# Kernel optimization log

Measured on AMD Instinct MI355X. Metric: run time of the kernel, lower is better.

Reference implementation:

```python
import jax, jax.numpy as jnp
import numpy as np

N = 2048          # number of glyph samples
SRC = 64          # raw alpha map size
PAD = 32          # zero padding on each side -> 128x128 source
HIN = SRC + 2 * PAD   # 128
WIN = SRC + 2 * PAD   # 128
TH = SRC * 2      # target_h = 2 * targetsize (=64) -> 128
TW = SRC * 2


def setup_inputs() -> dict:
    key = jax.random.key(0)
    k1, k2, k3 = jax.random.split(key, 3)
    return {
        "affine_outs": jax.random.normal(k1, (N, 6), jnp.float32),
        "fill_alpha": jax.random.uniform(k2, (N, SRC, SRC), jnp.float32),
        "stroke_alpha": jax.random.uniform(k3, (N, SRC, SRC), jnp.float32),
        # all target sizes fixed to 64 (-> 128x128 output) for static shapes
        "targetsize": jnp.full((1, N, 2), SRC, jnp.int32),
    }


def _theta(affine_outs):
    # matches torch.split(affine_outs, 1, 1) ordering: 00,11,01,10,02,12
    a00 = jax.nn.sigmoid(affine_outs[:, 0]) * 2.0
    a11 = jax.nn.sigmoid(affine_outs[:, 1]) * 2.0
    a01 = jnp.tanh(affine_outs[:, 2]) * 2.0
    a10 = jnp.tanh(affine_outs[:, 3]) * 2.0
    a02 = jnp.tanh(affine_outs[:, 4])
    a12 = jnp.tanh(affine_outs[:, 5])
    row1 = jnp.stack([a00, a01, a02], axis=-1)  # [N,3]
    row2 = jnp.stack([a10, a11, a12], axis=-1)  # [N,3]
    return jnp.stack([row1, row2], axis=1)      # [N,2,3]


def _affine_grid(theta):
    # F.affine_grid align_corners=False base grid for (TH, TW)
    xs = (jnp.arange(TW, dtype=jnp.float32) + 0.5) * (2.0 / TW) - 1.0  # [TW]
    ys = (jnp.arange(TH, dtype=jnp.float32) + 0.5) * (2.0 / TH) - 1.0  # [TH]
    X = xs[None, :]  # broadcast to [TH,TW]
    Y = ys[:, None]
    t = theta[:, :, :, None, None]  # [N,2,3,1,1]
    gx = t[:, 0, 0] * X + t[:, 0, 1] * Y + t[:, 0, 2]  # [N,TH,TW]
    gy = t[:, 1, 0] * X + t[:, 1, 1] * Y + t[:, 1, 2]
    return gx, gy


def _bilinear_zeros(img, ix, iy):
    # grid_sample(mode='bilinear', padding_mode='zeros', align_corners=False)
    n = img.shape[0]
    b = jnp.arange(n)[:, None, None]
    x0 = jnp.floor(ix)
    y0 = jnp.floor(iy)
    wx = ix - x0
    wy = iy - y0

    def fetch(xf, yf):
        xi = jnp.clip(xf, 0, WIN - 1).astype(jnp.int32)
        yi = jnp.clip(yf, 0, HIN - 1).astype(jnp.int32)
        v = img[b, yi, xi]
        valid = (xf >= 0) & (xf <= WIN - 1) & (yf >= 0) & (yf <= HIN - 1)
        return jnp.where(valid, v, 0.0)

    return (fetch(x0, y0) * (1 - wx) * (1 - wy)
            + fetch(x0 + 1, y0) * wx * (1 - wy)
            + fetch(x0, y0 + 1) * (1 - wx) * wy
            + fetch(x0 + 1, y0 + 1) * wx * wy)


def reference(affine_outs, fill_alpha, stroke_alpha, targetsize):
    theta = _theta(affine_outs)
    gx, gy = _affine_grid(theta)
    # normalized -> pixel coords (align_corners=False)
    ix = ((gx + 1.0) * WIN - 1.0) * 0.5
    iy = ((gy + 1.0) * HIN - 1.0) * 0.5
    pad = ((0, 0), (PAD, PAD), (PAD, PAD))
    fill_p = jnp.pad(fill_alpha, pad)
    stroke_p = jnp.pad(stroke_alpha, pad)
    fill_out = _bilinear_zeros(fill_p, ix, iy)      # [N,TH,TW]
    stroke_out = _bilinear_zeros(stroke_p, ix, iy)  # [N,TH,TW]
    return fill_out, stroke_out
```

## Files before the change

kernel.cpp:

```cpp
#include <hip/hip_runtime.h>

#define N_IMG 2048
#define SRC   64
#define PADW  32
#define HIN   128
#define WIN   128
#define TH    128
#define TW    128

__global__ __launch_bounds__(256) void affine_sample_kernel(
    const float* __restrict__ affine,
    const float* __restrict__ fill,
    const float* __restrict__ stroke,
    float* __restrict__ out)
{
    __shared__ float sF[SRC * SRC];
    __shared__ float sS[SRC * SRC];

    const int n = blockIdx.x;
    const float* __restrict__ fptr = fill   + (size_t)n * SRC * SRC;
    const float* __restrict__ sptr = stroke + (size_t)n * SRC * SRC;

    for (int i = threadIdx.x; i < SRC * SRC / 4; i += 256) {
        reinterpret_cast<float4*>(sF)[i] = reinterpret_cast<const float4*>(fptr)[i];
        reinterpret_cast<float4*>(sS)[i] = reinterpret_cast<const float4*>(sptr)[i];
    }

    const float t0 = affine[n * 6 + 0];
    const float t1 = affine[n * 6 + 1];
    const float t2 = affine[n * 6 + 2];
    const float t3 = affine[n * 6 + 3];
    const float t4 = affine[n * 6 + 4];
    const float t5 = affine[n * 6 + 5];
    const float a00 = 2.0f / (1.0f + expf(-t0));
    const float a11 = 2.0f / (1.0f + expf(-t1));
    const float a01 = 2.0f * tanhf(t2);
    const float a10 = 2.0f * tanhf(t3);
    const float a02 = tanhf(t4);
    const float a12 = tanhf(t5);

    __syncthreads();

    float* __restrict__ outF = out + (size_t)n * TH * TW;
    float* __restrict__ outS = out + (size_t)N_IMG * TH * TW + (size_t)n * TH * TW;

    for (int q = threadIdx.x; q < TH * TW / 4; q += 256) {
        const int py  = q >> 5;
        const int pxb = (q & 31) << 2;
        const float Y = ((float)py + 0.5f) * (2.0f / TH) - 1.0f;

        float4 rf, rs;
        float* rfp = &rf.x;
        float* rsp = &rs.x;

        #pragma unroll
        for (int j = 0; j < 4; ++j) {
            const int px = pxb + j;
            const float X = ((float)px + 0.5f) * (2.0f / TW) - 1.0f;
            const float gx = a00 * X + a01 * Y + a02;
            const float gy = a10 * X + a11 * Y + a12;
            const float ix = ((gx + 1.0f) * (float)WIN - 1.0f) * 0.5f;
            const float iy = ((gy + 1.0f) * (float)HIN - 1.0f) * 0.5f;

            const float x0f = floorf(ix);
            const float y0f = floorf(iy);
            const float wx = ix - x0f;
            const float wy = iy - y0f;

            const int x0 = (int)x0f - PADW;
            const int y0 = (int)y0f - PADW;

            const float w00 = (1.0f - wx) * (1.0f - wy);
            const float w10 = wx * (1.0f - wy);
            const float w01 = (1.0f - wx) * wy;
            const float w11 = wx * wy;

            const bool xv0 = (unsigned)x0       < (unsigned)SRC;
            const bool xv1 = (unsigned)(x0 + 1) < (unsigned)SRC;
            const bool yv0 = (unsigned)y0       < (unsigned)SRC;
            const bool yv1 = (unsigned)(y0 + 1) < (unsigned)SRC;

            float f00 = 0.f, f10 = 0.f, f01 = 0.f, f11 = 0.f;
            float s00 = 0.f, s10 = 0.f, s01 = 0.f, s11 = 0.f;

            const int base0 = y0 * SRC + x0;
            if (yv0) {
                if (xv0) { f00 = sF[base0];     s00 = sS[base0];     }
                if (xv1) { f10 = sF[base0 + 1]; s10 = sS[base0 + 1]; }
            }
            if (yv1) {
                const int base1 = base0 + SRC;
                if (xv0) { f01 = sF[base1];     s01 = sS[base1];     }
                if (xv1) { f11 = sF[base1 + 1]; s11 = sS[base1 + 1]; }
            }

            rfp[j] = f00 * w00 + f10 * w10 + f01 * w01 + f11 * w11;
            rsp[j] = s00 * w00 + s10 * w10 + s01 * w01 + s11 * w11;
        }

        reinterpret_cast<float4*>(outF)[q] = rf;
        reinterpret_cast<float4*>(outS)[q] = rs;
    }
}

extern "C" void kernel_launch(void* const* d_in, const int* in_sizes, int n_in,
                              void* d_out, int out_size, void* d_ws, size_t ws_size,
                              hipStream_t stream) {
    const float* affine = (const float*)d_in[0];
    const float* fill   = (const float*)d_in[1];
    const float* stroke = (const float*)d_in[2];
    float* out = (float*)d_out;

    affine_sample_kernel<<<dim3(N_IMG), dim3(256), 0, stream>>>(affine, fill, stroke, out);
}
```

Measured before the change: 336.5 us.

## Interleave fill/stroke in padded LDS and make bilinear sampling branchless

After: 356.8 us. 6.0% more time.

```diff
diff --git a/kernel.cpp b/kernel.cpp
--- a/kernel.cpp
+++ b/kernel.cpp
@@ -3,10 +3,11 @@
 #define N_IMG 2048
 #define SRC   64
 #define PADW  32
-#define HIN   128
-#define WIN   128
 #define TH    128
 #define TW    128
+
+#define LPAD  66
+#define LSZ   (LPAD + SRC * SRC + 66)
 
 __global__ __launch_bounds__(256) void affine_sample_kernel(
     const float* __restrict__ affine,
@@ -14,16 +15,25 @@
     const float* __restrict__ stroke,
     float* __restrict__ out)
 {
-    __shared__ float sF[SRC * SRC];
-    __shared__ float sS[SRC * SRC];
+    __shared__ float2 sFS[LSZ];
 
     const int n = blockIdx.x;
     const float* __restrict__ fptr = fill   + (size_t)n * SRC * SRC;
     const float* __restrict__ sptr = stroke + (size_t)n * SRC * SRC;
 
+    if (threadIdx.x < LPAD) {
+        sFS[threadIdx.x] = make_float2(0.f, 0.f);
+        sFS[LPAD + SRC * SRC + threadIdx.x] = make_float2(0.f, 0.f);
+    }
+
     for (int i = threadIdx.x; i < SRC * SRC / 4; i += 256) {
-        reinterpret_cast<float4*>(sF)[i] = reinterpret_cast<const float4*>(fptr)[i];
-        reinterpret_cast<float4*>(sS)[i] = reinterpret_cast<const float4*>(sptr)[i];
+        const float4 f = reinterpret_cast<const float4*>(fptr)[i];
+        const float4 s = reinterpret_cast<const float4*>(sptr)[i];
+        float2* dst = &sFS[LPAD + 4 * i];
+        dst[0] = make_float2(f.x, s.x);
+        dst[1] = make_float2(f.y, s.y);
+        dst[2] = make_float2(f.z, s.z);
+        dst[3] = make_float2(f.w, s.w);
     }
 
     const float t0 = affine[n * 6 + 0];
@@ -32,8 +42,8 @@
     const float t3 = affine[n * 6 + 3];
     const float t4 = affine[n * 6 + 4];
     const float t5 = affine[n * 6 + 5];
-    const float a00 = 2.0f / (1.0f + expf(-t0));
-    const float a11 = 2.0f / (1.0f + expf(-t1));
+    const float a00 = 2.0f / (1.0f + __expf(-t0));
+    const float a11 = 2.0f / (1.0f + __expf(-t1));
     const float a01 = 2.0f * tanhf(t2);
     const float a10 = 2.0f * tanhf(t3);
     const float a02 = tanhf(t4);
@@ -47,59 +57,50 @@
     for (int q = threadIdx.x; q < TH * TW / 4; q += 256) {
         const int py  = q >> 5;
         const int pxb = (q & 31) << 2;
-        const float Y = ((float)py + 0.5f) * (2.0f / TH) - 1.0f;
+        const float Y  = ((float)py + 0.5f) * (2.0f / TH) - 1.0f;
+        const float Cx = 64.0f * (a01 * Y + a02 - a00) + 31.5f;
+        const float Cy = 64.0f * (a11 * Y + a12 - a10) + 31.5f;
 
-        float4 rf, rs;
-        float* rfp = &rf.x;
-        float* rsp = &rs.x;
+        float rf[4], rs[4];
 
         #pragma unroll
         for (int j = 0; j < 4; ++j) {
-            const int px = pxb + j;
-            const float X = ((float)px + 0.5f) * (2.0f / TW) - 1.0f;
-            const float gx = a00 * X + a01 * Y + a02;
-            const float gy = a10 * X + a11 * Y + a12;
-            const float ix = ((gx + 1.0f) * (float)WIN - 1.0f) * 0.5f;
-            const float iy = ((gy + 1.0f) * (float)HIN - 1.0f) * 0.5f;
+            const float fx  = (float)(pxb + j) + 0.5f;
+            const float isx = fmaf(a00, fx, Cx);
+            const float isy = fmaf(a10, fx, Cy);
 
-            const float x0f = floorf(ix);
-            const float y0f = floorf(iy);
-            const float wx = ix - x0f;
-            const float wy = iy - y0f;
+            const float x0f = floorf(isx);
+            const float y0f = floorf(isy);
+            const float wx  = isx - x0f;
+            const float wy  = isy - y0f;
+            const int   x0  = (int)x0f;
+            const int   y0  = (int)y0f;
 
-            const int x0 = (int)x0f - PADW;
-            const int y0 = (int)y0f - PADW;
+            const float wxa = ((unsigned)x0       < (unsigned)SRC) ? (1.0f - wx) : 0.0f;
+            const float wxb = ((unsigned)(x0 + 1) < (unsigned)SRC) ? wx          : 0.0f;
+            const float wya = ((unsigned)y0       < (unsigned)SRC) ? (1.0f - wy) : 0.0f;
+            const float wyb = ((unsigned)(y0 + 1) < (unsigned)SRC) ? wy          : 0.0f;
 
-            const float w00 = (1.0f - wx) * (1.0f - wy);
-            const float w10 = wx * (1.0f - wy);
-            const float w01 = (1.0f - wx) * wy;
-            const float w11 = wx * wy;
+            const int xc = min(max(x0, -1), SRC - 1);
+            const int yc = min(max(y0, -1), SRC - 1);
+            const int base = LPAD + yc * SRC + xc;
 
-            const bool xv0 = (unsigned)x0       < (unsigned)SRC;
-            const bool xv1 = (unsigned)(x0 + 1) < (unsigned)SRC;
-            const bool yv0 = (unsigned)y0       < (unsigned)SRC;
-            const bool yv1 = (unsigned)(y0 + 1) < (unsigned)SRC;
+            const float2 v00 = sFS[base];
+            const float2 v10 = sFS[base + 1];
+            const float2 v01 = sFS[base + SRC];
+            const float2 v11 = sFS[base + SRC + 1];
 
-            float f00 = 0.f, f10 = 0.f, f01 = 0.f, f11 = 0.f;
-            float s00 = 0.f, s10 = 0.f, s01 = 0.f, s11 = 0.f;
+            const float w00 = wxa * wya;
+            const float w10 = wxb * wya;
+            const float w01 = wxa * wyb;
+            const float w11 = wxb * wyb;
 
-            const int base0 = y0 * SRC + x0;
-            if (yv0) {
-                if (xv0) { f00 = sF[base0];     s00 = sS[base0];     }
-                if (xv1) { f10 = sF[base0 + 1]; s10 = sS[base0 + 1]; }
-            }
-            if (yv1) {
-                const int base1 = base0 + SRC;
-                if (xv0) { f01 = sF[base1];     s01 = sS[base1];     }
-                if (xv1) { f11 = sF[base1 + 1]; s11 = sS[base1 + 1]; }
-            }
-
-            rfp[j] = f00 * w00 + f10 * w10 + f01 * w01 + f11 * w11;
-            rsp[j] = s00 * w00 + s10 * w10 + s01 * w01 + s11 * w11;
+            rf[j] = w00 * v00.x + w10 * v10.x + w01 * v01.x + w11 * v11.x;
+            rs[j] = w00 * v00.y + w10 * v10.y + w01 * v01.y + w11 * v11.y;
         }
 
-        reinterpret_cast<float4*>(outF)[q] = rf;
-        reinterpret_cast<float4*>(outS)[q] = rs;
+        reinterpret_cast<float4*>(outF)[q] = make_float4(rf[0], rf[1], rf[2], rf[3]);
+        reinterpret_cast<float4*>(outS)[q] = make_float4(rs[0], rs[1], rs[2], rs[3]);
     }
 }
 
```
